# Optimization experiments

Hardware: AMD Instinct MI355X
Metric: run time of the kernel (lower is better)

Reference implementation:

```python
import jax, jax.numpy as jnp
import numpy as np

ORDER = 3
N_LANES = 5  # lane ids 1..5 (0 = background)
EPS_DEN = 1e-5
RIDGE = 1e-6  # tiny jitter so the 4x4 normal-equation solve is well-posed (matches lstsq on full-rank data)


def setup_inputs() -> dict:
    key = jax.random.key(0)
    k1, k2 = jax.random.split(key)
    hnet_params = jax.random.normal(k1, (8, 6), dtype=jnp.float32)
    instance_label = jax.random.randint(k2, (8, 256, 512), 0, N_LANES + 1).astype(jnp.int64)
    return {"hnet_params": hnet_params, "instance_label": instance_label}


def reference(hnet_params, instance_label):
    B, Hh, Ww = instance_label.shape
    N = Hh * Ww
    p = hnet_params
    z = jnp.zeros((B,), p.dtype)
    o = jnp.ones((B,), p.dtype)
    # H = [[p0,p1,p2],[0,p3,p4],[0,p5,1]]
    Hm = jnp.stack([
        jnp.stack([p[:, 0], p[:, 1], p[:, 2]], -1),
        jnp.stack([z, p[:, 3], p[:, 4]], -1),
        jnp.stack([z, p[:, 5], o], -1),
    ], axis=1)  # [B,3,3]

    yy, xx = jnp.meshgrid(jnp.arange(Hh), jnp.arange(Ww), indexing='ij')
    P = jnp.stack([xx.reshape(-1), yy.reshape(-1), jnp.ones((N,), jnp.int32)]).astype(jnp.float32)  # [3,N]
    Pp = jnp.einsum('bij,jn->bin', Hm, P)  # [B,3,N]
    den = Pp[:, 2]
    den = jnp.where(jnp.abs(den) < EPS_DEN, jnp.full_like(den, EPS_DEN), den)
    xp = Pp[:, 0] / den  # [B,N]
    yp = Pp[:, 1] / den  # [B,N]

    exps = jnp.arange(ORDER, -1, -1)  # powers order..0
    Y = yp[..., None] ** exps  # [B,N,k]

    lane_ids = jnp.arange(1, N_LANES + 1)
    m = (instance_label.reshape(B, 1, N) == lane_ids[None, :, None]).astype(jnp.float32)  # [B,L,N]
    cnt = m.sum(-1)  # [B,L]
    cnt_safe = jnp.maximum(cnt, 1.0)

    # weighted normal equations per (batch, lane): (Y^T M Y) w = Y^T M x'
    A = jnp.einsum('bln,bni,bnj->blij', m, Y, Y)
    rhs = jnp.einsum('bln,bni,bn->bli', m, Y, xp)
    k = ORDER + 1
    A = A + RIDGE * jnp.eye(k, dtype=A.dtype)
    w = jnp.linalg.solve(A, rhs[..., None])[..., 0]  # [B,L,k]

    x_pred = jnp.einsum('bni,bli->bln', Y, w)  # [B,L,N]
    mse = (m * (xp[:, None, :] - x_pred) ** 2).sum(-1) / cnt_safe
    mad = (m * jnp.abs(den)[:, None, :]).sum(-1) / cnt_safe
    lane_loss = mse * mad  # [B,L]

    valid = (cnt >= ORDER + 1).astype(jnp.float32)
    nv = valid.sum()
    loss = jnp.where(nv > 0, (valid * lane_loss).sum() / jnp.maximum(nv, 1.0), 0.0)
    return loss
```

## Files before the change

kernel.cpp:

```cpp
#include <hip/hip_runtime.h>

#define BB 8
#define HH 256
#define WW 512
#define NLANES 5
#define KORD 4
#define RIDGE_D 1e-6
#define EPS_DEN_F 1e-5f

#define STATS_INTS (BB * NLANES * HH * 3)

__global__ void row_hist_kernel(const int* __restrict__ labels,
                                int* __restrict__ stats,
                                double* __restrict__ acc,
                                unsigned int* __restrict__ counter) {
    if (blockIdx.x == 0 && threadIdx.x == 0) {
        acc[0] = 0.0;
        acc[1] = 0.0;
        *counter = 0u;
    }

    const int row  = blockIdx.x;
    const int lane = threadIdx.x;
    const int* rp = labels + (size_t)row * WW;

    int c[NLANES], sx[NLANES], sxx[NLANES];
#pragma unroll
    for (int l = 0; l < NLANES; ++l) { c[l] = 0; sx[l] = 0; sxx[l] = 0; }

#pragma unroll
    for (int h = 0; h < 2; ++h) {
        const int j0 = h * 256 + lane * 4;
        const int4 v = *reinterpret_cast<const int4*>(rp + j0);
        const int vv[4] = {v.x, v.y, v.z, v.w};
#pragma unroll
        for (int q = 0; q < 4; ++q) {
            const int j   = j0 + q;
            const int lab = vv[q];
#pragma unroll
            for (int l = 0; l < NLANES; ++l) {
                const int mm = (lab == l + 1) ? 1 : 0;
                c[l]   += mm;
                sx[l]  += mm * j;
                sxx[l] += mm * j * j;
            }
        }
    }

#pragma unroll
    for (int l = 0; l < NLANES; ++l) {
#pragma unroll
        for (int off = 32; off > 0; off >>= 1) {
            c[l]   += __shfl_down(c[l],   off);
            sx[l]  += __shfl_down(sx[l],  off);
            sxx[l] += __shfl_down(sxx[l], off);
        }
    }

    if (lane == 0) {
        const int b = row >> 8;
        const int i = row & 255;
#pragma unroll
        for (int l = 0; l < NLANES; ++l) {
            int* o = stats + (((b * NLANES + l) * HH + i) * 3);
            o[0] = c[l]; o[1] = sx[l]; o[2] = sxx[l];
        }
    }
}

__global__ void lane_fit_kernel(const float* __restrict__ hp,
                                const int* __restrict__ stats,
                                double* __restrict__ acc,
                                unsigned int* __restrict__ counter,
                                float* __restrict__ out) {
    const int blk  = blockIdx.x;
    const int b    = blk / NLANES;
    const int l    = blk % NLANES;
    const int lane = threadIdx.x;

    const float p0 = hp[b * 6 + 0];
    const float p1 = hp[b * 6 + 1];
    const float p2 = hp[b * 6 + 2];
    const float p3 = hp[b * 6 + 3];
    const float p4 = hp[b * 6 + 4];
    const float p5 = hp[b * 6 + 5];

    const int* sb = stats + ((b * NLANES + l) * HH) * 3;

    double A[10];
    double r[4];
    double mad = 0.0, cnt = 0.0;
#pragma unroll
    for (int u = 0; u < 10; ++u) A[u] = 0.0;
#pragma unroll
    for (int u = 0; u < 4; ++u)  r[u] = 0.0;

#pragma unroll
    for (int k = 0; k < 4; ++k) {
        const int i = lane + 64 * k;
        const float yf = (float)i;
        float den = p5 * yf + 1.0f;
        if (fabsf(den) < EPS_DEN_F) den = EPS_DEN_F;
        const float ypf = (p3 * yf + p4) / den;
        const float qf  = p1 * yf + p2;

        const double dend = (double)den;
        const double yp   = (double)ypf;
        const double Yv[4] = { yp * yp * yp, yp * yp, yp, 1.0 };

        const int* s = sb + i * 3;
        const double cd  = (double)s[0];
        const double sxd = (double)s[1];
        const double a0  = (double)p0 / dend;
        const double bq  = (double)qf / dend;
        const double rw  = a0 * sxd + bq * cd;

        int idx = 0;
#pragma unroll
        for (int u = 0; u < 4; ++u)
#pragma unroll
            for (int v2 = u; v2 < 4; ++v2)
                A[idx++] += cd * Yv[u] * Yv[v2];
#pragma unroll
        for (int u = 0; u < 4; ++u) r[u] += Yv[u] * rw;

        mad += cd * fabs(dend);
        cnt += cd;
    }

#pragma unroll
    for (int u = 0; u < 10; ++u)
#pragma unroll
        for (int off = 32; off > 0; off >>= 1) A[u] += __shfl_xor(A[u], off);
#pragma unroll
    for (int u = 0; u < 4; ++u)
#pragma unroll
        for (int off = 32; off > 0; off >>= 1) r[u] += __shfl_xor(r[u], off);
#pragma unroll
    for (int off = 32; off > 0; off >>= 1) { mad += __shfl_xor(mad, off);
                                             cnt += __shfl_xor(cnt, off); }

    double m00 = A[0] + RIDGE_D, m01 = A[1],           m02 = A[2],           m03 = A[3];
    double m11 = A[4] + RIDGE_D, m12 = A[5],           m13 = A[6];
    double m22 = A[7] + RIDGE_D, m23 = A[8];
    double m33 = A[9] + RIDGE_D;
    double r0 = r[0], r1 = r[1], r2 = r[2], r3 = r[3];

    const double inv0 = 1.0 / m00;
    {
        const double f10 = m01 * inv0, f20 = m02 * inv0, f30 = m03 * inv0;
        m11 -= f10 * m01; m12 -= f10 * m02; m13 -= f10 * m03;
        m22 -= f20 * m02; m23 -= f20 * m03;
        m33 -= f30 * m03;
        r1  -= f10 * r0;  r2  -= f20 * r0;  r3  -= f30 * r0;
    }
    const double inv1 = 1.0 / m11;
    {
        const double f21 = m12 * inv1, f31 = m13 * inv1;
        m22 -= f21 * m12; m23 -= f21 * m13;
        m33 -= f31 * m13;
        r2  -= f21 * r1;  r3  -= f31 * r1;
    }
    const double inv2 = 1.0 / m22;
    {
        const double f32v = m23 * inv2;
        m33 -= f32v * m23;
        r3  -= f32v * r2;
    }
    const double w3 = (m33 != 0.0) ? r3 / m33 : 0.0;
    const double w2 = (r2 - m23 * w3) * inv2;
    const double w1 = (r1 - m12 * w2 - m13 * w3) * inv1;
    const double w0 = (r0 - m01 * w1 - m02 * w2 - m03 * w3) * inv0;

    double msesum = 0.0;
#pragma unroll
    for (int k = 0; k < 4; ++k) {
        const int i = lane + 64 * k;
        const float yf = (float)i;
        float den = p5 * yf + 1.0f;
        if (fabsf(den) < EPS_DEN_F) den = EPS_DEN_F;
        const float ypf = (p3 * yf + p4) / den;
        const float qf  = p1 * yf + p2;

        const double dend = (double)den;
        const double yp   = (double)ypf;
        const int* s = sb + i * 3;
        const double cd   = (double)s[0];
        const double sxd  = (double)s[1];
        const double sxxd = (double)s[2];
        const double a0   = (double)p0 / dend;
        const double bq   = (double)qf / dend;

        const double t = ((w0 * yp + w1) * yp + w2) * yp + w3;
        const double e = bq - t;
        msesum += a0 * a0 * sxxd + 2.0 * a0 * e * sxd + e * e * cd;
    }
#pragma unroll
    for (int off = 32; off > 0; off >>= 1) msesum += __shfl_down(msesum, off);

    if (lane == 0) {
        const double cnt_safe = fmax(cnt, 1.0);
        const double mse = msesum / cnt_safe;
        const double mdm = mad / cnt_safe;
        const double ll  = mse * mdm;
        const double vv  = (cnt >= (double)KORD) ? 1.0 : 0.0;

        atomicAdd(&acc[0], vv * ll);
        atomicAdd(&acc[1], vv);
        __threadfence();
        const unsigned int prev = atomicAdd(counter, 1u);
        if (prev == (unsigned int)(BB * NLANES - 1)) {
            const double num = atomicAdd(&acc[0], 0.0);
            const double nv  = atomicAdd(&acc[1], 0.0);
            const double loss = (nv > 0.0) ? num / fmax(nv, 1.0) : 0.0;
            out[0] = (float)loss;
        }
    }
}

extern "C" void kernel_launch(void* const* d_in, const int* in_sizes, int n_in,
                              void* d_out, int out_size, void* d_ws, size_t ws_size,
                              hipStream_t stream) {
    const float* hp     = (const float*)d_in[0];
    const int*   labels = (const int*)d_in[1];
    float*       out    = (float*)d_out;

    int*          stats   = (int*)d_ws;
    double*       acc     = (double*)((char*)d_ws + STATS_INTS * sizeof(int));
    unsigned int* counter = (unsigned int*)(acc + 2);

    row_hist_kernel<<<BB * HH, 64, 0, stream>>>(labels, stats, acc, counter);
    lane_fit_kernel<<<BB * NLANES, 64, 0, stream>>>(hp, stats, acc, counter, out);
}
```

Before: 15.40 us.

## Fuse per-row stats into moment accumulation and compute MSE via closed-form residual

The histogram kernel now processes 16 rows per 512-thread block and immediately converts per-row lane statistics into 13 power-moment partial sums (Y powers up to 6, the right-hand side, the x'^2 term and the mad term). A single-block finalize kernel sums the partials, solves the 4x4 system, and gets the weighted squared error algebraically as sum x'^2 - w·r - ridge·|w|^2 instead of a second pass over rows. This removes the per-row stats round trip, the second evaluation loop and the global atomics/counter. In exchange the MSE is now a difference of large terms, which risks cancellation error, clamped at zero.

```diff
diff --git a/kernel.cpp b/kernel.cpp
--- a/kernel.cpp
+++ b/kernel.cpp
@@ -4,39 +4,44 @@
 #define HH 256
 #define WW 512
 #define NLANES 5
-#define KORD 4
 #define RIDGE_D 1e-6
 #define EPS_DEN_F 1e-5f
 
-#define STATS_INTS (BB * NLANES * HH * 3)
-
-__global__ void row_hist_kernel(const int* __restrict__ labels,
-                                int* __restrict__ stats,
-                                double* __restrict__ acc,
-                                unsigned int* __restrict__ counter) {
-    if (blockIdx.x == 0 && threadIdx.x == 0) {
-        acc[0] = 0.0;
-        acc[1] = 0.0;
-        *counter = 0u;
-    }
-
-    const int row  = blockIdx.x;
-    const int lane = threadIdx.x;
-    const int* rp = labels + (size_t)row * WW;
+#define RG_PER_B 16
+#define ROWS_PG  16
+#define NBLK     (BB * RG_PER_B)
+#define NPART    13
+
+__global__ __launch_bounds__(512) void hist_acc_kernel(
+        const int* __restrict__ labels,
+        const float* __restrict__ hp,
+        double* __restrict__ part) {
+    const int bp = blockIdx.x;
+    const int b  = bp >> 4;
+    const int rg = bp & 15;
+    const int t  = threadIdx.x;
+    const int r  = t >> 5;
+    const int ch = t & 31;
+
+    __shared__ int sm[ROWS_PG][16];
+
+    const int row_i = rg * ROWS_PG + r;
+    const int4* rp4 = reinterpret_cast<const int4*>(
+        labels + ((size_t)(b * HH + row_i)) * WW + ch * 16);
 
     int c[NLANES], sx[NLANES], sxx[NLANES];
 #pragma unroll
     for (int l = 0; l < NLANES; ++l) { c[l] = 0; sx[l] = 0; sxx[l] = 0; }
 
 #pragma unroll
-    for (int h = 0; h < 2; ++h) {
-        const int j0 = h * 256 + lane * 4;
-        const int4 v = *reinterpret_cast<const int4*>(rp + j0);
+    for (int q = 0; q < 4; ++q) {
+        const int4 v = rp4[q];
+        const int jb = ch * 16 + q * 4;
         const int vv[4] = {v.x, v.y, v.z, v.w};
 #pragma unroll
-        for (int q = 0; q < 4; ++q) {
-            const int j   = j0 + q;
-            const int lab = vv[q];
+        for (int e = 0; e < 4; ++e) {
+            const int lab = vv[e];
+            const int j   = jb + e;
 #pragma unroll
             for (int l = 0; l < NLANES; ++l) {
                 const int mm = (lab == l + 1) ? 1 : 0;
@@ -50,54 +55,34 @@
 #pragma unroll
     for (int l = 0; l < NLANES; ++l) {
 #pragma unroll
-        for (int off = 32; off > 0; off >>= 1) {
-            c[l]   += __shfl_down(c[l],   off);
-            sx[l]  += __shfl_down(sx[l],  off);
-            sxx[l] += __shfl_down(sxx[l], off);
-        }
-    }
-
-    if (lane == 0) {
-        const int b = row >> 8;
-        const int i = row & 255;
+        for (int off = 16; off > 0; off >>= 1) {
+            c[l]   += __shfl_xor(c[l],   off);
+            sx[l]  += __shfl_xor(sx[l],  off);
+            sxx[l] += __shfl_xor(sxx[l], off);
+        }
+    }
+    if (ch == 0) {
 #pragma unroll
         for (int l = 0; l < NLANES; ++l) {
-            int* o = stats + (((b * NLANES + l) * HH + i) * 3);
-            o[0] = c[l]; o[1] = sx[l]; o[2] = sxx[l];
-        }
-    }
-}
-
-__global__ void lane_fit_kernel(const float* __restrict__ hp,
-                                const int* __restrict__ stats,
-                                double* __restrict__ acc,
-                                unsigned int* __restrict__ counter,
-                                float* __restrict__ out) {
-    const int blk  = blockIdx.x;
-    const int b    = blk / NLANES;
-    const int l    = blk % NLANES;
-    const int lane = threadIdx.x;
-
-    const float p0 = hp[b * 6 + 0];
-    const float p1 = hp[b * 6 + 1];
-    const float p2 = hp[b * 6 + 2];
-    const float p3 = hp[b * 6 + 3];
-    const float p4 = hp[b * 6 + 4];
-    const float p5 = hp[b * 6 + 5];
-
-    const int* sb = stats + ((b * NLANES + l) * HH) * 3;
-
-    double A[10];
-    double r[4];
-    double mad = 0.0, cnt = 0.0;
-#pragma unroll
-    for (int u = 0; u < 10; ++u) A[u] = 0.0;
-#pragma unroll
-    for (int u = 0; u < 4; ++u)  r[u] = 0.0;
-
-#pragma unroll
-    for (int k = 0; k < 4; ++k) {
-        const int i = lane + 64 * k;
+            sm[r][3 * l + 0] = c[l];
+            sm[r][3 * l + 1] = sx[l];
+            sm[r][3 * l + 2] = sxx[l];
+        }
+    }
+    __syncthreads();
+
+    if (t < NLANES * ROWS_PG) {
+        const int l  = t >> 4;
+        const int rr = t & 15;
+        const int i  = rg * ROWS_PG + rr;
+
+        const float p0 = hp[b * 6 + 0];
+        const float p1 = hp[b * 6 + 1];
+        const float p2 = hp[b * 6 + 2];
+        const float p3 = hp[b * 6 + 3];
+        const float p4 = hp[b * 6 + 4];
+        const float p5 = hp[b * 6 + 5];
+
         const float yf = (float)i;
         float den = p5 * yf + 1.0f;
         if (fabsf(den) < EPS_DEN_F) den = EPS_DEN_F;
@@ -106,115 +91,120 @@
 
         const double dend = (double)den;
         const double yp   = (double)ypf;
-        const double Yv[4] = { yp * yp * yp, yp * yp, yp, 1.0 };
-
-        const int* s = sb + i * 3;
-        const double cd  = (double)s[0];
-        const double sxd = (double)s[1];
-        const double a0  = (double)p0 / dend;
-        const double bq  = (double)qf / dend;
-        const double rw  = a0 * sxd + bq * cd;
-
-        int idx = 0;
-#pragma unroll
-        for (int u = 0; u < 4; ++u)
-#pragma unroll
-            for (int v2 = u; v2 < 4; ++v2)
-                A[idx++] += cd * Yv[u] * Yv[v2];
-#pragma unroll
-        for (int u = 0; u < 4; ++u) r[u] += Yv[u] * rw;
-
-        mad += cd * fabs(dend);
-        cnt += cd;
-    }
-
-#pragma unroll
-    for (int u = 0; u < 10; ++u)
-#pragma unroll
-        for (int off = 32; off > 0; off >>= 1) A[u] += __shfl_xor(A[u], off);
-#pragma unroll
-    for (int u = 0; u < 4; ++u)
-#pragma unroll
-        for (int off = 32; off > 0; off >>= 1) r[u] += __shfl_xor(r[u], off);
-#pragma unroll
-    for (int off = 32; off > 0; off >>= 1) { mad += __shfl_xor(mad, off);
-                                             cnt += __shfl_xor(cnt, off); }
-
-    double m00 = A[0] + RIDGE_D, m01 = A[1],           m02 = A[2],           m03 = A[3];
-    double m11 = A[4] + RIDGE_D, m12 = A[5],           m13 = A[6];
-    double m22 = A[7] + RIDGE_D, m23 = A[8];
-    double m33 = A[9] + RIDGE_D;
-    double r0 = r[0], r1 = r[1], r2 = r[2], r3 = r[3];
-
-    const double inv0 = 1.0 / m00;
-    {
-        const double f10 = m01 * inv0, f20 = m02 * inv0, f30 = m03 * inv0;
-        m11 -= f10 * m01; m12 -= f10 * m02; m13 -= f10 * m03;
-        m22 -= f20 * m02; m23 -= f20 * m03;
-        m33 -= f30 * m03;
-        r1  -= f10 * r0;  r2  -= f20 * r0;  r3  -= f30 * r0;
-    }
-    const double inv1 = 1.0 / m11;
-    {
-        const double f21 = m12 * inv1, f31 = m13 * inv1;
-        m22 -= f21 * m12; m23 -= f21 * m13;
-        m33 -= f31 * m13;
-        r2  -= f21 * r1;  r3  -= f31 * r1;
-    }
-    const double inv2 = 1.0 / m22;
-    {
-        const double f32v = m23 * inv2;
-        m33 -= f32v * m23;
-        r3  -= f32v * r2;
-    }
-    const double w3 = (m33 != 0.0) ? r3 / m33 : 0.0;
-    const double w2 = (r2 - m23 * w3) * inv2;
-    const double w1 = (r1 - m12 * w2 - m13 * w3) * inv1;
-    const double w0 = (r0 - m01 * w1 - m02 * w2 - m03 * w3) * inv0;
-
-    double msesum = 0.0;
-#pragma unroll
-    for (int k = 0; k < 4; ++k) {
-        const int i = lane + 64 * k;
-        const float yf = (float)i;
-        float den = p5 * yf + 1.0f;
-        if (fabsf(den) < EPS_DEN_F) den = EPS_DEN_F;
-        const float ypf = (p3 * yf + p4) / den;
-        const float qf  = p1 * yf + p2;
-
-        const double dend = (double)den;
-        const double yp   = (double)ypf;
-        const int* s = sb + i * 3;
-        const double cd   = (double)s[0];
-        const double sxd  = (double)s[1];
-        const double sxxd = (double)s[2];
-        const double a0   = (double)p0 / dend;
-        const double bq   = (double)qf / dend;
-
-        const double t = ((w0 * yp + w1) * yp + w2) * yp + w3;
-        const double e = bq - t;
-        msesum += a0 * a0 * sxxd + 2.0 * a0 * e * sxd + e * e * cd;
-    }
-#pragma unroll
-    for (int off = 32; off > 0; off >>= 1) msesum += __shfl_down(msesum, off);
-
-    if (lane == 0) {
-        const double cnt_safe = fmax(cnt, 1.0);
-        const double mse = msesum / cnt_safe;
-        const double mdm = mad / cnt_safe;
-        const double ll  = mse * mdm;
-        const double vv  = (cnt >= (double)KORD) ? 1.0 : 0.0;
-
-        atomicAdd(&acc[0], vv * ll);
-        atomicAdd(&acc[1], vv);
-        __threadfence();
-        const unsigned int prev = atomicAdd(counter, 1u);
-        if (prev == (unsigned int)(BB * NLANES - 1)) {
-            const double num = atomicAdd(&acc[0], 0.0);
-            const double nv  = atomicAdd(&acc[1], 0.0);
-            const double loss = (nv > 0.0) ? num / fmax(nv, 1.0) : 0.0;
-            out[0] = (float)loss;
-        }
+        const double cd   = (double)sm[rr][3 * l + 0];
+        const double sxd  = (double)sm[rr][3 * l + 1];
+        const double sxxd = (double)sm[rr][3 * l + 2];
+
+        const double a0 = (double)p0 / dend;
+        const double bq = (double)qf / dend;
+        const double rw = a0 * sxd + bq * cd;
+
+        const double yp2 = yp * yp;
+        const double yp3 = yp2 * yp;
+        const double yp4 = yp2 * yp2;
+        const double yp5 = yp3 * yp2;
+        const double yp6 = yp3 * yp3;
+
+        double v[NPART];
+        v[0]  = cd;
+        v[1]  = cd * yp;
+        v[2]  = cd * yp2;
+        v[3]  = cd * yp3;
+        v[4]  = cd * yp4;
+        v[5]  = cd * yp5;
+        v[6]  = cd * yp6;
+        v[7]  = rw * yp3;
+        v[8]  = rw * yp2;
+        v[9]  = rw * yp;
+        v[10] = rw;
+        v[11] = a0 * a0 * sxxd + 2.0 * a0 * bq * sxd + bq * bq * cd;
+        v[12] = cd * fabs(dend);
+
+#pragma unroll
+        for (int u = 0; u < NPART; ++u)
+#pragma unroll
+            for (int off = 8; off > 0; off >>= 1)
+                v[u] += __shfl_xor(v[u], off);
+
+        if ((t & 15) == 0) {
+            double* o = part + ((size_t)(bp * NLANES + l)) * NPART;
+#pragma unroll
+            for (int u = 0; u < NPART; ++u) o[u] = v[u];
+        }
+    }
+}
+
+__global__ void solve_finalize_kernel(const double* __restrict__ part,
+                                      float* __restrict__ out) {
+    const int t = threadIdx.x;
+    double num = 0.0, nv = 0.0;
+
+    if (t < BB * NLANES) {
+        const int b = t / NLANES;
+        const int l = t % NLANES;
+
+        double v[NPART];
+#pragma unroll
+        for (int u = 0; u < NPART; ++u) v[u] = 0.0;
+        for (int rg = 0; rg < RG_PER_B; ++rg) {
+            const double* p =
+                part + ((size_t)((b * RG_PER_B + rg) * NLANES + l)) * NPART;
+#pragma unroll
+            for (int u = 0; u < NPART; ++u) v[u] += p[u];
+        }
+
+        double m00 = v[6] + RIDGE_D, m01 = v[5], m02 = v[4], m03 = v[3];
+        double m11 = v[4] + RIDGE_D, m12 = v[3], m13 = v[2];
+        double m22 = v[2] + RIDGE_D, m23 = v[1];
+        double m33 = v[0] + RIDGE_D;
+        double r0 = v[7], r1 = v[8], r2 = v[9], r3 = v[10];
+
+        const double inv0 = 1.0 / m00;
+        {
+            const double f10 = m01 * inv0, f20 = m02 * inv0, f30 = m03 * inv0;
+            m11 -= f10 * m01; m12 -= f10 * m02; m13 -= f10 * m03;
+            m22 -= f20 * m02; m23 -= f20 * m03;
+            m33 -= f30 * m03;
+            r1  -= f10 * r0;  r2  -= f20 * r0;  r3  -= f30 * r0;
+        }
+        const double inv1 = 1.0 / m11;
+        {
+            const double f21 = m12 * inv1, f31 = m13 * inv1;
+            m22 -= f21 * m12; m23 -= f21 * m13;
+            m33 -= f31 * m13;
+            r2  -= f21 * r1;  r3  -= f31 * r1;
+        }
+        const double inv2 = 1.0 / m22;
+        {
+            const double f32v = m23 * inv2;
+            m33 -= f32v * m23;
+            r3  -= f32v * r2;
+        }
+        const double w3 = (m33 != 0.0) ? r3 / m33 : 0.0;
+        const double w2 = (r2 - m23 * w3) * inv2;
+        const double w1 = (r1 - m12 * w2 - m13 * w3) * inv1;
+        const double w0 = (r0 - m01 * w1 - m02 * w2 - m03 * w3) * inv0;
+
+        const double wr  = w0 * v[7] + w1 * v[8] + w2 * v[9] + w3 * v[10];
+        const double ww  = w0 * w0 + w1 * w1 + w2 * w2 + w3 * w3;
+        const double msesum = fmax(v[11] - wr - RIDGE_D * ww, 0.0);
+
+        const double cnt = v[0];
+        const double cs  = fmax(cnt, 1.0);
+        const double ll  = (msesum / cs) * (v[12] / cs);
+        const double vv  = (cnt >= 4.0) ? 1.0 : 0.0;
+        num = vv * ll;
+        nv  = vv;
+    }
+
+#pragma unroll
+    for (int off = 32; off > 0; off >>= 1) {
+        num += __shfl_down(num, off);
+        nv  += __shfl_down(nv,  off);
+    }
+    if (t == 0) {
+        const double loss = (nv > 0.0) ? num / fmax(nv, 1.0) : 0.0;
+        out[0] = (float)loss;
     }
 }
 
@@ -225,10 +215,8 @@
     const int*   labels = (const int*)d_in[1];
     float*       out    = (float*)d_out;
 
-    int*          stats   = (int*)d_ws;
-    double*       acc     = (double*)((char*)d_ws + STATS_INTS * sizeof(int));
-    unsigned int* counter = (unsigned int*)(acc + 2);
-
-    row_hist_kernel<<<BB * HH, 64, 0, stream>>>(labels, stats, acc, counter);
-    lane_fit_kernel<<<BB * NLANES, 64, 0, stream>>>(hp, stats, acc, counter, out);
+    double* part = (double*)d_ws;
+
+    hist_acc_kernel<<<NBLK, 512, 0, stream>>>(labels, hp, part);
+    solve_finalize_kernel<<<1, 64, 0, stream>>>(part, out);
 }
```

Measured after the change: 17.06 us. 1.11x slower.
